# Kernel tuning notes

Measured on AMD Instinct MI355X. Metric: run time of the kernel, lower is better.

## Reference

```python
import jax, jax.numpy as jnp
import numpy as np

EPS = 1e-5
TEMP = 50.0


def setup_inputs() -> dict:
    key = jax.random.key(0)
    features = jax.random.normal(key, (4, 64, 128, 128), dtype=jnp.float32)
    return {"features": features, "patch_sim_neiref_neisimavgsize": 5}


def reference(features, patch_sim_neiref_neisimavgsize):
    k = patch_sim_neiref_neisimavgsize
    B, C, H, W = features.shape
    pad = k // 2
    xp = jnp.pad(features, ((0, 0), (0, 0), (pad, pad), (pad, pad)))
    # windows ordered (kh, kw) to match F.unfold: [B, k*k, C, H, W]
    wins = jnp.stack([xp[:, :, i:i + H, j:j + W]
                      for i in range(k) for j in range(k)], axis=1)
    # [B, H, W, k*k, C]
    patch = jnp.transpose(wins, (0, 3, 4, 1, 2)) + EPS
    patch_norm = patch / jnp.sqrt(jnp.sum(patch * patch, axis=-1, keepdims=True))
    center = patch_norm[..., (k * k) // 2:(k * k) // 2 + 1, :]  # center pixel of window
    sim = jnp.sum(patch_norm * center, axis=-1, keepdims=True)   # cosine sim [B,H,W,kk,1]
    wei = jax.nn.softmax(TEMP * sim, axis=-2)
    repr_vec = jnp.sum(patch * wei, axis=-2)                     # [B,H,W,C]
    return jnp.transpose(repr_vec, (0, 3, 1, 2))                 # [B,C,H,W]
```

## Files before the change

kernel.cpp:

```cpp
#include <hip/hip_runtime.h>

#define EPS 1e-5f
#define TEMP 50.0f
#define CCH 64
#define HH 128
#define WW 128
#define HWSZ (HH * WW)
#define CEPS2 (CCH * EPS * EPS)
#define K2E 72.13475204444817f

#define ITW 16
#define ITH 8
#define HTW 20
#define HTH 12
#define HPX (HTW * HTH)
#define HPAD 241

typedef _Float16 h16;
typedef h16 h2v __attribute__((ext_vector_type(2)));
typedef h16 h8v __attribute__((ext_vector_type(8)));
union H8 { h8v v; h2v p[4]; };

__device__ __forceinline__ float fdot2(h2v a, h2v b, float c) {
#if __has_builtin(__builtin_amdgcn_fdot2)
    return __builtin_amdgcn_fdot2(a, b, c, false);
#else
    return c + (float)a[0] * (float)b[0] + (float)a[1] * (float)b[1];
#endif
}

__device__ __forceinline__ h2v pkrtz(float a, float b) {
#if __has_builtin(__builtin_amdgcn_cvt_pkrtz)
    return __builtin_bit_cast(h2v, __builtin_amdgcn_cvt_pkrtz(a, b));
#else
    return (h2v){(h16)a, (h16)b};
#endif
}

__device__ __forceinline__ float fexp2(float x) {
#if __has_builtin(__builtin_amdgcn_exp2f)
    return __builtin_amdgcn_exp2f(x);
#else
    return exp2f(x);
#endif
}

__device__ __forceinline__ float frcp(float x) {
#if __has_builtin(__builtin_amdgcn_rcpf)
    return __builtin_amdgcn_rcpf(x);
#else
    return 1.f / x;
#endif
}

__device__ __forceinline__ float dpp_xor1(float x) {
#if __has_builtin(__builtin_amdgcn_mov_dpp)
    int i = __builtin_bit_cast(int, x);
    int a = __builtin_amdgcn_mov_dpp(i, 0xB1, 0xF, 0xF, true);
    return __builtin_bit_cast(float, a);
#else
    return __shfl_xor(x, 1);
#endif
}

__device__ __forceinline__ float quad_sum(float x) {
#if __has_builtin(__builtin_amdgcn_mov_dpp)
    float x1 = x + dpp_xor1(x);
    int j = __builtin_bit_cast(int, x1);
    int b = __builtin_amdgcn_mov_dpp(j, 0x4E, 0xF, 0xF, true);
    return x1 + __builtin_bit_cast(float, b);
#else
    float x1 = x + __shfl_xor(x, 1);
    return x1 + __shfl_xor(x1, 2);
#endif
}

#define TP_PAD 72
__global__ __launch_bounds__(256) void rv_transpose(const float* __restrict__ x,
                                                    h16* __restrict__ xt) {
    __shared__ h16 buf[WW][TP_PAD];
    const int t = threadIdx.x;
    const int h = blockIdx.x;
    const int b = blockIdx.y;
    const float* src = x + (size_t)b * (CCH * HWSZ) + h * WW;
#pragma unroll 4
    for (int i = 0; i < 16; ++i) {
        int k = i * 256 + t;
        int w  = k & 127;
        int cp = k >> 7;
        float v0 = src[(size_t)(2 * cp) * HWSZ + w];
        float v1 = src[(size_t)(2 * cp + 1) * HWSZ + w];
        *(h2v*)&buf[w][2 * cp] = pkrtz(v0, v1);
    }
    __syncthreads();
    h16* dst = xt + (size_t)(b * HH + h) * WW * CCH;
#pragma unroll
    for (int j = 0; j < 4; ++j) {
        int idx = j * 256 + t;
        int w = idx >> 3;
        int q = idx & 7;
        h8v v = *(const h8v*)&buf[w][q * 8];
        *(h8v*)&dst[(size_t)w * CCH + q * 8] = v;
    }
}

__global__ __launch_bounds__(512) void rv_fused(const h16* __restrict__ xt,
                                                float* __restrict__ out) {
    __shared__ h8v  tile[8][HPAD];
    __shared__ float sh_rn[HPX];

    const int t  = threadIdx.x;
    const int w0 = blockIdx.x * ITW;
    const int h0 = blockIdx.y * ITH;
    const int b  = blockIdx.z;

#pragma unroll
    for (int it = 0; it < 4; ++it) {
        int k = it * 512 + t;
        if (k < 8 * HPX) {
            int q  = k & 7;
            int px = k >> 3;
            int row = px / HTW;
            int col = px - row * HTW;
            int gh = h0 + row - 2;
            int gw = w0 + col - 2;
            h8v v = {};
            if ((unsigned)gh < (unsigned)HH && (unsigned)gw < (unsigned)WW) {
                v = *(const h8v*)&xt[((size_t)(b * HH + gh) * WW + gw) * CCH + q * 8];
            }
            tile[q][px] = v;
        }
    }
    __syncthreads();

    if (t < 2 * HPX) {
        const int px   = t >> 1;
        const int hbse = (t & 1) * 4;
        float q = 0.f;
#pragma unroll
        for (int hq = 0; hq < 4; ++hq) {
            H8 u; u.v = tile[hbse + hq][px];
#pragma unroll
            for (int j = 0; j < 4; ++j) q = fdot2(u.p[j], u.p[j], q);
        }
        const float qt = q + dpp_xor1(q);
        if (!(t & 1)) sh_rn[px] = rsqrtf(qt + CEPS2);
    }
    __syncthreads();

    const int qg  = t & 3;
    const int pix = t >> 2;
    const int r   = pix >> 4;
    const int cl  = pix & 15;
    const int cpx = (r + 2) * HTW + (cl + 2);

    const float rinvC2 = K2E * sh_rn[cpx];

    H8 ctr0, ctr1;
    ctr0.v = tile[2 * qg][cpx];
    ctr1.v = tile[2 * qg + 1][cpx];

    h2v acc[8] = {};
    float wsum = 0.f;

#pragma unroll
    for (int dr = 0; dr < 5; ++dr) {
#pragma unroll
        for (int dc = 0; dc < 5; ++dc) {
            const int npx = (r + dr) * HTW + (cl + dc);
            H8 a0, a1;
            a0.v = tile[2 * qg][npx];
            a1.v = tile[2 * qg + 1][npx];
            float d0 = 0.f, d1 = 0.f;
#pragma unroll
            for (int j = 0; j < 4; ++j) d0 = fdot2(ctr0.p[j], a0.p[j], d0);
#pragma unroll
            for (int j = 0; j < 4; ++j) d1 = fdot2(ctr1.p[j], a1.p[j], d1);
            float d = quad_sum(d0 + d1);
            const float u = (d + CEPS2) * sh_rn[npx];
            const float wn = fexp2(fmaf(u, rinvC2, -K2E));
            wsum += wn;
            const h16 wh = (h16)wn;
            const h2v w2 = {wh, wh};
#pragma unroll
            for (int j = 0; j < 4; ++j) {
                acc[j]     = a0.p[j] * w2 + acc[j];
                acc[4 + j] = a1.p[j] * w2 + acc[4 + j];
            }
        }
    }

    const float rs = frcp(wsum);
    const size_t obase = (size_t)b * (CCH * HWSZ)
                       + (size_t)(qg * 16) * HWSZ
                       + (h0 + r) * WW + (w0 + cl);
#pragma unroll
    for (int j = 0; j < 8; ++j) {
        const float f0 = (float)acc[j][0];
        const float f1 = (float)acc[j][1];
        out[obase + (size_t)(2 * j) * HWSZ]     = fmaf(f0, rs, EPS);
        out[obase + (size_t)(2 * j + 1) * HWSZ] = fmaf(f1, rs, EPS);
    }
}

extern "C" void kernel_launch(void* const* d_in, const int* in_sizes, int n_in,
                              void* d_out, int out_size, void* d_ws, size_t ws_size,
                              hipStream_t stream) {
    const float* x = (const float*)d_in[0];
    float* outp = (float*)d_out;
    h16* xt = (h16*)d_ws;

    rv_transpose<<<dim3(HH, 4), dim3(256), 0, stream>>>(x, xt);
    rv_fused<<<dim3(WW / ITW, HH / ITH, 4), dim3(512, 1, 1), 0, stream>>>(xt, outp);
}
```

Before: 79.51 us.

## Fuse fp16 transpose into main kernel, loading NCHW fp32 halo tiles directly

```diff
diff --git a/kernel.cpp b/kernel.cpp
--- a/kernel.cpp
+++ b/kernel.cpp
@@ -75,37 +75,8 @@
 #endif
 }
 
-#define TP_PAD 72
-__global__ __launch_bounds__(256) void rv_transpose(const float* __restrict__ x,
-                                                    h16* __restrict__ xt) {
-    __shared__ h16 buf[WW][TP_PAD];
-    const int t = threadIdx.x;
-    const int h = blockIdx.x;
-    const int b = blockIdx.y;
-    const float* src = x + (size_t)b * (CCH * HWSZ) + h * WW;
-#pragma unroll 4
-    for (int i = 0; i < 16; ++i) {
-        int k = i * 256 + t;
-        int w  = k & 127;
-        int cp = k >> 7;
-        float v0 = src[(size_t)(2 * cp) * HWSZ + w];
-        float v1 = src[(size_t)(2 * cp + 1) * HWSZ + w];
-        *(h2v*)&buf[w][2 * cp] = pkrtz(v0, v1);
-    }
-    __syncthreads();
-    h16* dst = xt + (size_t)(b * HH + h) * WW * CCH;
-#pragma unroll
-    for (int j = 0; j < 4; ++j) {
-        int idx = j * 256 + t;
-        int w = idx >> 3;
-        int q = idx & 7;
-        h8v v = *(const h8v*)&buf[w][q * 8];
-        *(h8v*)&dst[(size_t)w * CCH + q * 8] = v;
-    }
-}
-
-__global__ __launch_bounds__(512) void rv_fused(const h16* __restrict__ xt,
-                                                float* __restrict__ out) {
+__global__ __launch_bounds__(512) void rv_onepass(const float* __restrict__ x,
+                                                  float* __restrict__ out) {
     __shared__ h8v  tile[8][HPAD];
     __shared__ float sh_rn[HPX];
 
@@ -114,21 +85,32 @@
     const int h0 = blockIdx.y * ITH;
     const int b  = blockIdx.z;
 
+    {
+        const int wv = t >> 6;
+        const int l  = t & 63;
+        const float* xw = x + ((size_t)b * CCH + 8 * wv) * HWSZ;
+        h16* dstq = (h16*)&tile[wv][0];
 #pragma unroll
-    for (int it = 0; it < 4; ++it) {
-        int k = it * 512 + t;
-        if (k < 8 * HPX) {
-            int q  = k & 7;
-            int px = k >> 3;
-            int row = px / HTW;
-            int col = px - row * HTW;
-            int gh = h0 + row - 2;
-            int gw = w0 + col - 2;
-            h8v v = {};
-            if ((unsigned)gh < (unsigned)HH && (unsigned)gw < (unsigned)WW) {
-                v = *(const h8v*)&xt[((size_t)(b * HH + gh) * WW + gw) * CCH + q * 8];
+        for (int s = 0; s < 4; ++s) {
+            const int px = s * 64 + l;
+            if (px < HPX) {
+                const int row = px / HTW;
+                const int col = px - row * HTW;
+                const int gh  = h0 + row - 2;
+                const int gw  = w0 + col - 2;
+                const bool ok = (unsigned)gh < (unsigned)HH &&
+                                (unsigned)gw < (unsigned)WW;
+                const int off = gh * WW + gw;
+#pragma unroll
+                for (int j = 0; j < 4; ++j) {
+                    float v0 = 0.f, v1 = 0.f;
+                    if (ok) {
+                        v0 = xw[(size_t)(2 * j) * HWSZ + off];
+                        v1 = xw[(size_t)(2 * j + 1) * HWSZ + off];
+                    }
+                    *(h2v*)&dstq[px * 8 + 2 * j] = pkrtz(v0, v1);
+                }
             }
-            tile[q][px] = v;
         }
     }
     __syncthreads();
@@ -208,8 +190,7 @@
                               hipStream_t stream) {
     const float* x = (const float*)d_in[0];
     float* outp = (float*)d_out;
-    h16* xt = (h16*)d_ws;
+    (void)d_ws; (void)ws_size;
 
-    rv_transpose<<<dim3(HH, 4), dim3(256), 0, stream>>>(x, xt);
-    rv_fused<<<dim3(WW / ITW, HH / ITH, 4), dim3(512, 1, 1), 0, stream>>>(xt, outp);
+    rv_onepass<<<dim3(WW / ITW, HH / ITH, 4), dim3(512, 1, 1), 0, stream>>>(x, outp);
 }
```

After: 86.84 us. 1.09x slower.
